# Performance work log

Measured on AMD Instinct MI355X. Metric: run time of the kernel, lower is better.

The kernel has to match this reference:

```python
import jax, jax.numpy as jnp
import numpy as np

B = 4096      # graphs per batch
V = 32        # vertices per graph
F = 16        # num_atom_types (input node features)
NB = 8        # num_bond_types (edge feature dim)
C = 128       # conv_dim
E_PER = 256   # random edges per graph
NEG_SLOPE = 0.2


def setup_inputs() -> dict:
    rng = np.random.default_rng(0)
    N = B * V
    # random intra-graph edges (duplicates are fine; softmax handles them)
    off = (np.arange(B, dtype=np.int64) * V)[:, None]
    src = (rng.integers(0, V, (B, E_PER)) + off).ravel()
    dst = (rng.integers(0, V, (B, E_PER)) + off).ravel()
    bond = rng.integers(0, NB, src.shape[0])
    eattr = np.zeros((src.shape[0], NB), dtype=np.float32)
    eattr[np.arange(src.shape[0]), bond] = 1.0
    # self loops with edge_attr = per-target-node mean (PyG fill_value='mean')
    sums = np.zeros((N, NB), dtype=np.float64)
    np.add.at(sums, dst, eattr)
    cnt = np.bincount(dst, minlength=N).astype(np.float64)
    loop_attr = (sums / np.maximum(cnt, 1.0)[:, None]).astype(np.float32)
    loops = np.arange(N, dtype=np.int64)
    edge_index = np.stack([np.concatenate([src, loops]),
                           np.concatenate([dst, loops])])  # [2, E]
    edge_attr = np.concatenate([eattr, loop_attr], axis=0)  # [E, NB]

    key = jax.random.key(0)
    ks = jax.random.split(key, 8)
    inp = {
        "x": jax.random.normal(ks[0], (N, F), jnp.float32),
        "edge_index": jnp.asarray(edge_index),
        "edge_attr": jnp.asarray(edge_attr),
        "W_lin": jax.random.normal(ks[1], (F, C), jnp.float32) / np.sqrt(F),
        "att_src": jax.random.normal(ks[2], (C,), jnp.float32) / np.sqrt(C),
        "att_dst": jax.random.normal(ks[3], (C,), jnp.float32) / np.sqrt(C),
        "att_edge": jax.random.normal(ks[4], (C,), jnp.float32) / np.sqrt(C),
        "W_edge": jax.random.normal(ks[5], (NB, C), jnp.float32) / np.sqrt(NB),
        "b_gat": jnp.zeros((C,), jnp.float32),
        "W_out": jax.random.normal(ks[6], (C, 1), jnp.float32) / np.sqrt(C),
        "b_out": jnp.zeros((1,), jnp.float32),
        "num_graphs": B,
    }
    return inp


def reference(x, edge_index, edge_attr, W_lin, att_src, att_dst, att_edge,
              W_edge, b_gat, W_out, b_out, num_graphs):
    N = x.shape[0]
    src, dst = edge_index[0], edge_index[1]
    h = x @ W_lin                           # [N, C] node transform
    a_src = h @ att_src                     # [N]
    a_dst = h @ att_dst                     # [N]
    a_edge = (edge_attr @ W_edge) @ att_edge  # [E]
    alpha = jax.nn.leaky_relu(a_src[src] + a_dst[dst] + a_edge, NEG_SLOPE)
    # segment softmax over incoming edges of each dst node
    m = jax.ops.segment_max(alpha, dst, num_segments=N)
    m = jnp.where(jnp.isfinite(m), m, 0.0)
    ex = jnp.exp(alpha - m[dst])
    denom = jax.ops.segment_sum(ex, dst, num_segments=N)
    w = ex / denom[dst]                     # [E] attention weights
    msg = h[src] * w[:, None]               # [E, C]
    out_nodes = jax.ops.segment_sum(msg, dst, num_segments=N) + b_gat  # [N, C]
    gf = out_nodes.reshape(num_graphs, -1, out_nodes.shape[-1]).mean(axis=1)  # [B, C]
    out = gf @ W_out + b_out                # [B, 1]
    return (out, gf)
```

## Files before the change

kernel.cpp:

```cpp
#include <hip/hip_runtime.h>


#define BB   4096
#define VV   32
#define FF   16
#define NBB  8
#define CC   128
#define EPER 256
constexpr int NTOT  = BB * VV;
constexpr int ERAND = BB * EPER;
constexpr int ETOT  = ERAND + NTOT;
constexpr float SLOPE = 0.2f;

__launch_bounds__(64)
__global__ void gnn_precompute(const float* __restrict__ W_lin,
                               const float* __restrict__ att_src,
                               const float* __restrict__ att_dst,
                               const float* __restrict__ W_edge,
                               const float* __restrict__ att_edge,
                               float* __restrict__ ws)
{
  const int l = threadIdx.x;
  const float2 as = ((const float2*)att_src)[l];
  const float2 ad = ((const float2*)att_dst)[l];
  const float2 ae = ((const float2*)att_edge)[l];
  #pragma unroll
  for (int f = 0; f < FF; ++f) {
    const float2 w = ((const float2*)W_lin)[f * 64 + l];
    float ps = w.x * as.x + w.y * as.y;
    float pd = w.x * ad.x + w.y * ad.y;
    #pragma unroll
    for (int m = 1; m <= 32; m <<= 1) { ps += __shfl_xor(ps, m); pd += __shfl_xor(pd, m); }
    if (l == 0) { ws[f] = ps; ws[FF + f] = pd; }
  }
  #pragma unroll
  for (int f = 0; f < NBB; ++f) {
    const float2 w = ((const float2*)W_edge)[f * 64 + l];
    float pe = w.x * ae.x + w.y * ae.y;
    #pragma unroll
    for (int m = 1; m <= 32; m <<= 1) pe += __shfl_xor(pe, m);
    if (l == 0) ws[2 * FF + f] = pe;
  }
}

__launch_bounds__(256, 4)
__global__ void gnn_main(const float* __restrict__ x,
                         const int*   __restrict__ eidx,
                         const float* __restrict__ eattr,
                         const float* __restrict__ W_lin,
                         const float* __restrict__ b_gat,
                         const float* __restrict__ W_out,
                         const float* __restrict__ b_out,
                         const float* __restrict__ ws,
                         float* __restrict__ out,
                         float* __restrict__ gf_out)
{
  const int t    = threadIdx.x;
  const int lane = t & 63;
  const int wave = __builtin_amdgcn_readfirstlane(t) >> 6;
  const int g    = blockIdx.x * 4 + wave;

  __shared__ float s_asrc[4][VV], s_adst[4][VV];
  __shared__ float s_den[4][VV];
  __shared__ float s_r[4][VV];
  __shared__ float s_xt[4][FF * 33];

  if (lane < VV) { s_den[wave][lane] = 0.f; s_r[wave][lane] = 0.f; }

  float xr[FF] = {};
  if (lane < VV) {
    const float* xp = x + (size_t)(g * VV + lane) * FF;
    #pragma unroll
    for (int f = 0; f < FF; ++f) xr[f] = xp[f];
  }

  int es[4], ed[4];
  const int4 s4 = ((const int4*)(eidx + g * EPER))[lane];
  const int4 d4 = ((const int4*)(eidx + ETOT + g * EPER))[lane];
  es[0] = s4.x - g * VV; es[1] = s4.y - g * VV; es[2] = s4.z - g * VV; es[3] = s4.w - g * VV;
  ed[0] = d4.x - g * VV; ed[1] = d4.y - g * VV; ed[2] = d4.z - g * VV; ed[3] = d4.w - g * VV;
  float4 ea[8];
  {
    const float4* ap = (const float4*)(eattr + (size_t)(g * EPER + 4 * lane) * NBB);
    #pragma unroll
    for (int j = 0; j < 8; ++j) ea[j] = ap[j];
  }
  float4 la0 = {0,0,0,0}, la1 = {0,0,0,0};
  if (lane >= VV) {
    const float4* lp = (const float4*)(eattr + (size_t)(ERAND + g * VV + (lane - VV)) * NBB);
    la0 = lp[0]; la1 = lp[1];
  }

  if (lane < VV) {
    float a0 = 0.f, a1 = 0.f;
    #pragma unroll
    for (int f = 0; f < FF; ++f) { a0 += xr[f] * ws[f]; a1 += xr[f] * ws[FF + f]; }
    s_asrc[wave][lane] = a0; s_adst[wave][lane] = a1;
  }
  __threadfence_block();

  const float w0 = ws[32], w1 = ws[33], w2 = ws[34], w3 = ws[35];
  const float w4 = ws[36], w5 = ws[37], w6 = ws[38], w7 = ws[39];
  float ex[5];
  #pragma unroll
  for (int k = 0; k < 4; ++k) {
    const float aed = ea[2*k].x*w0 + ea[2*k].y*w1 + ea[2*k].z*w2 + ea[2*k].w*w3
                    + ea[2*k+1].x*w4 + ea[2*k+1].y*w5 + ea[2*k+1].z*w6 + ea[2*k+1].w*w7;
    const float a  = s_asrc[wave][es[k]] + s_adst[wave][ed[k]] + aed;
    const float al = a > 0.f ? a : SLOPE * a;
    ex[k] = __expf(al);
    atomicAdd(&s_den[wave][ed[k]], ex[k]);
  }
  ex[4] = 0.f;
  if (lane >= VV) {
    const int v = lane - VV;
    const float aed = la0.x*w0 + la0.y*w1 + la0.z*w2 + la0.w*w3
                    + la1.x*w4 + la1.y*w5 + la1.z*w6 + la1.w*w7;
    const float a  = s_asrc[wave][v] + s_adst[wave][v] + aed;
    const float al = a > 0.f ? a : SLOPE * a;
    ex[4] = __expf(al);
    atomicAdd(&s_den[wave][v], ex[4]);
  }
  __threadfence_block();

  #pragma unroll
  for (int k = 0; k < 4; ++k)
    atomicAdd(&s_r[wave][es[k]], ex[k] * __builtin_amdgcn_rcpf(s_den[wave][ed[k]]));
  if (lane >= VV) {
    const int v = lane - VV;
    atomicAdd(&s_r[wave][v], ex[4] * __builtin_amdgcn_rcpf(s_den[wave][v]));
  }
  __threadfence_block();

  if (lane < VV) {
    const float rl = s_r[wave][lane];
    #pragma unroll
    for (int f = 0; f < FF; ++f) s_xt[wave][f * 33 + lane] = xr[f] * rl;
  }
  __threadfence_block();
  const int fy = lane & 15, part = lane >> 4;
  float yp = 0.f;
  #pragma unroll
  for (int j = 0; j < 8; ++j) yp += s_xt[wave][fy * 33 + part * 8 + j];
  yp += __shfl_xor(yp, 16);
  yp += __shfl_xor(yp, 32);
  yp *= (1.0f / VV);

  const float2 bg = ((const float2*)b_gat)[lane];
  float gx = bg.x, gy = bg.y;
  const float2* W2 = (const float2*)W_lin;
  #pragma unroll
  for (int f = 0; f < FF; ++f) {
    const float yf = __shfl(yp, f);
    const float2 w = W2[f * 64 + lane];
    gx += yf * w.x; gy += yf * w.y;
  }
  ((float2*)(gf_out + (size_t)g * CC))[lane] = make_float2(gx, gy);

  const float2 wo = ((const float2*)W_out)[lane];
  float p = gx * wo.x + gy * wo.y;
  #pragma unroll
  for (int m = 1; m <= 32; m <<= 1) p += __shfl_xor(p, m);
  if (lane == 0) out[g] = p + b_out[0];
}

extern "C" void kernel_launch(void* const* d_in, const int* in_sizes, int n_in,
                              void* d_out, int out_size, void* d_ws, size_t ws_size,
                              hipStream_t stream) {
  const float* x        = (const float*)d_in[0];
  const int*   eidx     = (const int*)  d_in[1];
  const float* eattr    = (const float*)d_in[2];
  const float* W_lin    = (const float*)d_in[3];
  const float* att_src  = (const float*)d_in[4];
  const float* att_dst  = (const float*)d_in[5];
  const float* att_edge = (const float*)d_in[6];
  const float* W_edge   = (const float*)d_in[7];
  const float* b_gat    = (const float*)d_in[8];
  const float* W_out    = (const float*)d_in[9];
  const float* b_out    = (const float*)d_in[10];

  float* ws  = (float*)d_ws;
  float* out = (float*)d_out;
  float* gf  = out + BB;

  gnn_precompute<<<dim3(1), dim3(64), 0, stream>>>(W_lin, att_src, att_dst,
                                                   W_edge, att_edge, ws);
  gnn_main<<<dim3(BB / 4), dim3(256), 0, stream>>>(
      x, eidx, eattr, W_lin, b_gat, W_out, b_out, ws, out, gf);
}
```

Baseline: 128.6 us.

## Fuse weight precompute into main kernel and coalesce edge loads

```diff
diff --git a/kernel.cpp b/kernel.cpp
--- a/kernel.cpp
+++ b/kernel.cpp
@@ -12,111 +12,123 @@
 constexpr int ETOT  = ERAND + NTOT;
 constexpr float SLOPE = 0.2f;
 
-__launch_bounds__(64)
-__global__ void gnn_precompute(const float* __restrict__ W_lin,
-                               const float* __restrict__ att_src,
-                               const float* __restrict__ att_dst,
-                               const float* __restrict__ W_edge,
-                               const float* __restrict__ att_edge,
-                               float* __restrict__ ws)
-{
-  const int l = threadIdx.x;
-  const float2 as = ((const float2*)att_src)[l];
-  const float2 ad = ((const float2*)att_dst)[l];
-  const float2 ae = ((const float2*)att_edge)[l];
-  #pragma unroll
-  for (int f = 0; f < FF; ++f) {
-    const float2 w = ((const float2*)W_lin)[f * 64 + l];
-    float ps = w.x * as.x + w.y * as.y;
-    float pd = w.x * ad.x + w.y * ad.y;
-    #pragma unroll
-    for (int m = 1; m <= 32; m <<= 1) { ps += __shfl_xor(ps, m); pd += __shfl_xor(pd, m); }
-    if (l == 0) { ws[f] = ps; ws[FF + f] = pd; }
-  }
-  #pragma unroll
-  for (int f = 0; f < NBB; ++f) {
-    const float2 w = ((const float2*)W_edge)[f * 64 + l];
-    float pe = w.x * ae.x + w.y * ae.y;
-    #pragma unroll
-    for (int m = 1; m <= 32; m <<= 1) pe += __shfl_xor(pe, m);
-    if (l == 0) ws[2 * FF + f] = pe;
-  }
-}
-
 __launch_bounds__(256, 4)
-__global__ void gnn_main(const float* __restrict__ x,
-                         const int*   __restrict__ eidx,
-                         const float* __restrict__ eattr,
-                         const float* __restrict__ W_lin,
-                         const float* __restrict__ b_gat,
-                         const float* __restrict__ W_out,
-                         const float* __restrict__ b_out,
-                         const float* __restrict__ ws,
-                         float* __restrict__ out,
-                         float* __restrict__ gf_out)
+__global__ void gnn_all(const float* __restrict__ x,
+                        const int*   __restrict__ eidx,
+                        const float* __restrict__ eattr,
+                        const float* __restrict__ W_lin,
+                        const float* __restrict__ att_src,
+                        const float* __restrict__ att_dst,
+                        const float* __restrict__ att_edge,
+                        const float* __restrict__ W_edge,
+                        const float* __restrict__ b_gat,
+                        const float* __restrict__ W_out,
+                        const float* __restrict__ b_out,
+                        float* __restrict__ out,
+                        float* __restrict__ gf_out)
 {
   const int t    = threadIdx.x;
   const int lane = t & 63;
   const int wave = __builtin_amdgcn_readfirstlane(t) >> 6;
   const int g    = blockIdx.x * 4 + wave;
-
-  __shared__ float s_asrc[4][VV], s_adst[4][VV];
-  __shared__ float s_den[4][VV];
-  __shared__ float s_r[4][VV];
-  __shared__ float s_xt[4][FF * 33];
-
-  if (lane < VV) { s_den[wave][lane] = 0.f; s_r[wave][lane] = 0.f; }
-
-  float xr[FF] = {};
-  if (lane < VV) {
-    const float* xp = x + (size_t)(g * VV + lane) * FF;
-    #pragma unroll
-    for (int f = 0; f < FF; ++f) xr[f] = xp[f];
-  }
-
+  const int half = lane >> 5;
+  const int v    = lane & 31;
+
+  __shared__ float2 s_a[4][VV];
+  __shared__ float  s_den[4][VV];
+  __shared__ float  s_r[4][VV];
+  __shared__ float2 s_uv[4][FF];
+  __shared__ __align__(16) float s_we[4][NBB];
+  __shared__ float  s_xt[4][FF * 33];
+  __shared__ __align__(16) float s_y[4][FF];
+
+  float4 xa, xb;
+  {
+    const float* xp = x + (size_t)(g * VV + v) * FF + half * 8;
+    xa = ((const float4*)xp)[0]; xb = ((const float4*)xp)[1];
+  }
   int es[4], ed[4];
-  const int4 s4 = ((const int4*)(eidx + g * EPER))[lane];
-  const int4 d4 = ((const int4*)(eidx + ETOT + g * EPER))[lane];
-  es[0] = s4.x - g * VV; es[1] = s4.y - g * VV; es[2] = s4.z - g * VV; es[3] = s4.w - g * VV;
-  ed[0] = d4.x - g * VV; ed[1] = d4.y - g * VV; ed[2] = d4.z - g * VV; ed[3] = d4.w - g * VV;
-  float4 ea[8];
-  {
-    const float4* ap = (const float4*)(eattr + (size_t)(g * EPER + 4 * lane) * NBB);
-    #pragma unroll
-    for (int j = 0; j < 8; ++j) ea[j] = ap[j];
+  float4 ea0[4], ea1[4];
+  #pragma unroll
+  for (int k = 0; k < 4; ++k) {
+    const int e = g * EPER + 64 * k + lane;
+    es[k] = eidx[e] - g * VV;
+    ed[k] = eidx[ETOT + e] - g * VV;
+    const float4* ap = (const float4*)(eattr + (size_t)e * NBB);
+    ea0[k] = ap[0]; ea1[k] = ap[1];
   }
   float4 la0 = {0,0,0,0}, la1 = {0,0,0,0};
-  if (lane >= VV) {
-    const float4* lp = (const float4*)(eattr + (size_t)(ERAND + g * VV + (lane - VV)) * NBB);
+  if (half) {
+    const float4* lp = (const float4*)(eattr + (size_t)(ERAND + g * VV + v) * NBB);
     la0 = lp[0]; la1 = lp[1];
   }
 
-  if (lane < VV) {
-    float a0 = 0.f, a1 = 0.f;
-    #pragma unroll
-    for (int f = 0; f < FF; ++f) { a0 += xr[f] * ws[f]; a1 += xr[f] * ws[FF + f]; }
-    s_asrc[wave][lane] = a0; s_adst[wave][lane] = a1;
-  }
-  __threadfence_block();
-
-  const float w0 = ws[32], w1 = ws[33], w2 = ws[34], w3 = ws[35];
-  const float w4 = ws[36], w5 = ws[37], w6 = ws[38], w7 = ws[39];
+  {
+    const int fu = lane & 15, q = lane >> 4;
+    const float4* wr = (const float4*)(W_lin + fu * CC + q * 32);
+    const float4* as = (const float4*)(att_src + q * 32);
+    const float4* ad = (const float4*)(att_dst + q * 32);
+    float us = 0.f, ud = 0.f;
+    #pragma unroll
+    for (int j = 0; j < 8; ++j) {
+      const float4 w = wr[j], a = as[j], d = ad[j];
+      us += w.x*a.x + w.y*a.y + w.z*a.z + w.w*a.w;
+      ud += w.x*d.x + w.y*d.y + w.z*d.z + w.w*d.w;
+    }
+    us += __shfl_xor(us, 16); us += __shfl_xor(us, 32);
+    ud += __shfl_xor(ud, 16); ud += __shfl_xor(ud, 32);
+    if (lane < FF) s_uv[wave][lane] = make_float2(us, ud);
+  }
+  if (!half) {
+    const int f8 = v & 7, oct = v >> 3;
+    const float4* wr = (const float4*)(W_edge + f8 * CC + oct * 32);
+    const float4* ae = (const float4*)(att_edge + oct * 32);
+    float pe = 0.f;
+    #pragma unroll
+    for (int j = 0; j < 8; ++j) {
+      const float4 w = wr[j], a = ae[j];
+      pe += w.x*a.x + w.y*a.y + w.z*a.z + w.w*a.w;
+    }
+    pe += __shfl_xor(pe, 8); pe += __shfl_xor(pe, 16);
+    if (v < NBB) s_we[wave][v] = pe;
+  }
+
+  float a0 = 0.f, a1 = 0.f;
+  {
+    const float xr[8] = {xa.x, xa.y, xa.z, xa.w, xb.x, xb.y, xb.z, xb.w};
+    #pragma unroll
+    for (int j = 0; j < 8; ++j) {
+      const float2 u = s_uv[wave][half * 8 + j];
+      a0 += xr[j] * u.x; a1 += xr[j] * u.y;
+    }
+  }
+  a0 += __shfl_xor(a0, 32); a1 += __shfl_xor(a1, 32);
+  if (!half) {
+    s_a[wave][v] = make_float2(a0, a1);
+    s_den[wave][v] = 0.f; s_r[wave][v] = 0.f;
+  }
+  __threadfence_block();
+
+  const float4 w03 = *(const float4*)&s_we[wave][0];
+  const float4 w47 = *(const float4*)&s_we[wave][4];
   float ex[5];
   #pragma unroll
   for (int k = 0; k < 4; ++k) {
-    const float aed = ea[2*k].x*w0 + ea[2*k].y*w1 + ea[2*k].z*w2 + ea[2*k].w*w3
-                    + ea[2*k+1].x*w4 + ea[2*k+1].y*w5 + ea[2*k+1].z*w6 + ea[2*k+1].w*w7;
-    const float a  = s_asrc[wave][es[k]] + s_adst[wave][ed[k]] + aed;
+    const float2 A = s_a[wave][es[k]];
+    const float2 D = s_a[wave][ed[k]];
+    const float aed = ea0[k].x*w03.x + ea0[k].y*w03.y + ea0[k].z*w03.z + ea0[k].w*w03.w
+                    + ea1[k].x*w47.x + ea1[k].y*w47.y + ea1[k].z*w47.z + ea1[k].w*w47.w;
+    const float a  = A.x + D.y + aed;
     const float al = a > 0.f ? a : SLOPE * a;
     ex[k] = __expf(al);
     atomicAdd(&s_den[wave][ed[k]], ex[k]);
   }
   ex[4] = 0.f;
-  if (lane >= VV) {
-    const int v = lane - VV;
-    const float aed = la0.x*w0 + la0.y*w1 + la0.z*w2 + la0.w*w3
-                    + la1.x*w4 + la1.y*w5 + la1.z*w6 + la1.w*w7;
-    const float a  = s_asrc[wave][v] + s_adst[wave][v] + aed;
+  if (half) {
+    const float2 S = s_a[wave][v];
+    const float aed = la0.x*w03.x + la0.y*w03.y + la0.z*w03.z + la0.w*w03.w
+                    + la1.x*w47.x + la1.y*w47.y + la1.z*w47.z + la1.w*w47.w;
+    const float a  = S.x + S.y + aed;
     const float al = a > 0.f ? a : SLOPE * a;
     ex[4] = __expf(al);
     atomicAdd(&s_den[wave][v], ex[4]);
@@ -126,34 +138,41 @@
   #pragma unroll
   for (int k = 0; k < 4; ++k)
     atomicAdd(&s_r[wave][es[k]], ex[k] * __builtin_amdgcn_rcpf(s_den[wave][ed[k]]));
-  if (lane >= VV) {
-    const int v = lane - VV;
+  if (half)
     atomicAdd(&s_r[wave][v], ex[4] * __builtin_amdgcn_rcpf(s_den[wave][v]));
-  }
-  __threadfence_block();
-
-  if (lane < VV) {
-    const float rl = s_r[wave][lane];
-    #pragma unroll
-    for (int f = 0; f < FF; ++f) s_xt[wave][f * 33 + lane] = xr[f] * rl;
-  }
-  __threadfence_block();
-  const int fy = lane & 15, part = lane >> 4;
-  float yp = 0.f;
-  #pragma unroll
-  for (int j = 0; j < 8; ++j) yp += s_xt[wave][fy * 33 + part * 8 + j];
-  yp += __shfl_xor(yp, 16);
-  yp += __shfl_xor(yp, 32);
-  yp *= (1.0f / VV);
-
+  __threadfence_block();
+
+  {
+    const float rl = s_r[wave][v];
+    const float xr[8] = {xa.x, xa.y, xa.z, xa.w, xb.x, xb.y, xb.z, xb.w};
+    #pragma unroll
+    for (int j = 0; j < 8; ++j)
+      s_xt[wave][(half * 8 + j) * 33 + v] = xr[j] * rl;
+  }
+  __threadfence_block();
+  {
+    const int fy = lane & 15, part = lane >> 4;
+    float yp = 0.f;
+    #pragma unroll
+    for (int j = 0; j < 8; ++j) yp += s_xt[wave][fy * 33 + part * 8 + j];
+    yp += __shfl_xor(yp, 16); yp += __shfl_xor(yp, 32);
+    if (lane < FF) s_y[wave][lane] = yp * (1.0f / VV);
+  }
+  __threadfence_block();
+
+  const float4 y03 = *(const float4*)&s_y[wave][0];
+  const float4 y47 = *(const float4*)&s_y[wave][4];
+  const float4 y8b = *(const float4*)&s_y[wave][8];
+  const float4 ycf = *(const float4*)&s_y[wave][12];
+  const float yv[16] = {y03.x,y03.y,y03.z,y03.w, y47.x,y47.y,y47.z,y47.w,
+                        y8b.x,y8b.y,y8b.z,y8b.w, ycf.x,ycf.y,ycf.z,ycf.w};
   const float2 bg = ((const float2*)b_gat)[lane];
   float gx = bg.x, gy = bg.y;
   const float2* W2 = (const float2*)W_lin;
   #pragma unroll
   for (int f = 0; f < FF; ++f) {
-    const float yf = __shfl(yp, f);
     const float2 w = W2[f * 64 + lane];
-    gx += yf * w.x; gy += yf * w.y;
+    gx += yv[f] * w.x; gy += yv[f] * w.y;
   }
   ((float2*)(gf_out + (size_t)g * CC))[lane] = make_float2(gx, gy);
 
@@ -179,12 +198,10 @@
   const float* W_out    = (const float*)d_in[9];
   const float* b_out    = (const float*)d_in[10];
 
-  float* ws  = (float*)d_ws;
   float* out = (float*)d_out;
   float* gf  = out + BB;
 
-  gnn_precompute<<<dim3(1), dim3(64), 0, stream>>>(W_lin, att_src, att_dst,
-                                                   W_edge, att_edge, ws);
-  gnn_main<<<dim3(BB / 4), dim3(256), 0, stream>>>(
-      x, eidx, eattr, W_lin, b_gat, W_out, b_out, ws, out, gf);
+  gnn_all<<<dim3(BB / 4), dim3(256), 0, stream>>>(
+      x, eidx, eattr, W_lin, att_src, att_dst, att_edge, W_edge,
+      b_gat, W_out, b_out, out, gf);
 }
```

Measured after the change: 117.5 us. 8.6% less time.
